# Kernel optimization log

Hardware: AMD Instinct MI355X
Metric: run time of the kernel (lower is better)

Reference implementation:

```python
import jax, jax.numpy as jnp
import numpy as np

N = 100000
E = 1600000
F = 128
HID = 64
OUT = 64
LSTM_H = (3 * HID) // 2  # 96, PyG JumpingKnowledge lstm hidden size


def setup_inputs() -> dict:
    key = jax.random.key(0)
    ks = jax.random.split(key, 40)

    def w(k, shape, s=0.05):
        return jax.random.normal(k, shape, dtype=jnp.float32) * s

    inp = {}
    inp['x'] = jax.random.normal(ks[0], (N, F), dtype=jnp.float32)
    inp['edge_index'] = jax.random.randint(ks[1], (2, E), 0, N)
    # GINConv MLPs: Linear(in,hid) -> ReLU -> Linear(hid,hid)
    dims = [(F, HID), (HID, HID), (HID, HID)]
    for i, (a, b) in enumerate(dims):
        inp[f'W{i}a'] = w(ks[2 + 4 * i], (b, a))
        inp[f'b{i}a'] = w(ks[3 + 4 * i], (b,))
        inp[f'W{i}b'] = w(ks[4 + 4 * i], (b, b))
        inp[f'b{i}b'] = w(ks[5 + 4 * i], (b,))
    # JK bidirectional LSTM (torch gate order i,f,g,o)
    for j, d in enumerate(['f', 'b']):
        inp[f'Wih_{d}'] = w(ks[14 + 4 * j], (4 * LSTM_H, HID))
        inp[f'Whh_{d}'] = w(ks[15 + 4 * j], (4 * LSTM_H, LSTM_H))
        inp[f'bih_{d}'] = w(ks[16 + 4 * j], (4 * LSTM_H,))
        inp[f'bhh_{d}'] = w(ks[17 + 4 * j], (4 * LSTM_H,))
    inp['Watt'] = w(ks[22], (1, 2 * LSTM_H))
    inp['batt'] = w(ks[23], (1,))
    inp['Wlin'] = w(ks[24], (OUT, HID))
    inp['blin'] = w(ks[25], (OUT,))
    inp['Wfc1'] = w(ks[26], (1, OUT))
    inp['bfc1'] = w(ks[27], (1,))
    inp['Wfc2'] = w(ks[28], (1, N))
    inp['bfc2'] = w(ks[29], (1,))
    return inp


def _gin_layer(h, src, dst, Wa, ba, Wb, bb):
    # GINConv with eps=0: MLP((1+eps)*x + sum_{j in N(i)} x_j)
    agg = jax.ops.segment_sum(h[src], dst, num_segments=h.shape[0])
    z = h + agg
    z = jnp.maximum(z @ Wa.T + ba, 0.0)
    return z @ Wb.T + bb


def _lstm_scan(seq, Wih, Whh, bih, bhh):
    # seq: [L, N, C]; returns hidden states [L, N, H]
    H = Whh.shape[1]
    bias = bih + bhh

    def cell(carry, xt):
        hp, cp = carry
        g = xt @ Wih.T + hp @ Whh.T + bias
        i, f, gg, o = jnp.split(g, 4, axis=-1)
        c = jax.nn.sigmoid(f) * cp + jax.nn.sigmoid(i) * jnp.tanh(gg)
        hn = jax.nn.sigmoid(o) * jnp.tanh(c)
        return (hn, c), hn

    n = seq.shape[1]
    init = (jnp.zeros((n, H), seq.dtype), jnp.zeros((n, H), seq.dtype))
    _, hs = jax.lax.scan(cell, init, seq)
    return hs


def reference(x, edge_index, W0a, b0a, W0b, b0b, W1a, b1a, W1b, b1b,
              W2a, b2a, W2b, b2b, Wih_f, Whh_f, bih_f, bhh_f,
              Wih_b, Whh_b, bih_b, bhh_b, Watt, batt, Wlin, blin,
              Wfc1, bfc1, Wfc2, bfc2):
    src, dst = edge_index[0], edge_index[1]
    h = x
    xs = []
    for (Wa, ba, Wb, bb) in [(W0a, b0a, W0b, b0b), (W1a, b1a, W1b, b1b),
                             (W2a, b2a, W2b, b2b)]:
        h = _gin_layer(h, src, dst, Wa, ba, Wb, bb)
        h = jnp.maximum(h, 0.0)  # BasicGNN act (relu); dropout=identity in eval
        xs.append(h)
    seq = jnp.stack(xs, axis=0)  # [L, N, HID]
    hf = _lstm_scan(seq, Wih_f, Whh_f, bih_f, bhh_f)
    hb = _lstm_scan(seq[::-1], Wih_b, Whh_b, bih_b, bhh_b)[::-1]
    ao = jnp.concatenate([hf, hb], axis=-1)  # [L, N, 2*LSTM_H]
    alpha = (ao @ Watt.T + batt)[..., 0]  # [L, N]
    alpha = jax.nn.softmax(alpha, axis=0)  # softmax over layers
    xjk = jnp.einsum('lnc,ln->nc', seq, alpha)  # [N, HID]
    xo = xjk @ Wlin.T + blin  # [N, OUT]
    v = (xo @ Wfc1.T + bfc1)[:, 0]  # [N]
    v = jnp.where(v >= 0, v, 0.01 * v)  # LeakyReLU
    return Wfc2 @ v + bfc2  # [1]
```

## Files before the change

kernel.cpp:

```cpp
#include <hip/hip_runtime.h>
#include <stdint.h>

typedef unsigned short u16;
typedef unsigned int u32;
using short8 = __attribute__((ext_vector_type(8))) short;
using f32x16 = __attribute__((ext_vector_type(16))) float;

__device__ __forceinline__ float sigf(float x){
  return __builtin_amdgcn_rcpf(1.0f + __expf(-x));
}
__device__ __forceinline__ float tanh_f(float x){
  return 1.0f - 2.0f*__builtin_amdgcn_rcpf(1.0f + __expf(2.0f*x));
}
__device__ __forceinline__ u16 f2bf(float f){
  u32 u = __float_as_uint(f);
  u += 0x7FFFu + ((u>>16)&1u);
  return (u16)(u>>16);
}
__device__ __forceinline__ float bf2f(u16 h){ return __uint_as_float(((u32)h)<<16); }

__global__ void k_deg(const int* __restrict__ dst, int* __restrict__ deg, int E){
  int i = blockIdx.x*256 + threadIdx.x;
  if (i < E) atomicAdd(&deg[dst[i]], 1);
}

__global__ __launch_bounds__(256) void k_scan1(const int* __restrict__ deg, int* __restrict__ indptr,
                                               int* __restrict__ bsum, int N){
  __shared__ int s[256];
  int tid = threadIdx.x;
  int i = blockIdx.x*256 + tid;
  int v = (i < N) ? deg[i] : 0;
  s[tid] = v; __syncthreads();
  for (int off=1; off<256; off<<=1){
    int t = (tid>=off) ? s[tid-off] : 0;
    __syncthreads();
    s[tid] += t;
    __syncthreads();
  }
  if (i < N) indptr[i] = s[tid] - v;
  if (tid == 255) bsum[blockIdx.x] = s[255];
}

__global__ __launch_bounds__(512) void k_scan2(const int* __restrict__ bsum, int* __restrict__ boffs,
                                               int* __restrict__ indptr, int nb, int N){
  __shared__ int s[512];
  int tid = threadIdx.x;
  int v = (tid < nb) ? bsum[tid] : 0;
  s[tid] = v; __syncthreads();
  for (int off=1; off<512; off<<=1){
    int t = (tid>=off) ? s[tid-off] : 0;
    __syncthreads();
    s[tid] += t;
    __syncthreads();
  }
  boffs[tid] = s[tid] - v;
  if (tid == nb-1) indptr[N] = s[tid];
}

__global__ __launch_bounds__(256) void k_scan3(int* __restrict__ indptr, const int* __restrict__ boffs, int N){
  int i = blockIdx.x*256 + threadIdx.x;
  if (i < N) indptr[i] += boffs[blockIdx.x];
}

__global__ void k_fill(const int* __restrict__ src, const int* __restrict__ dst,
                       const int* __restrict__ indptr, int* __restrict__ fill,
                       int* __restrict__ col, int E){
  int i = blockIdx.x*256 + threadIdx.x;
  if (i < E){
    int d = dst[i];
    int r = atomicAdd(&fill[d], 1);
    col[indptr[d] + r] = src[i];
  }
}

template<int F>
__global__ __launch_bounds__(256) void k_agg(const float* __restrict__ y, const int* __restrict__ indptr,
                                             const int* __restrict__ col, const float* __restrict__ bias,
                                             float* __restrict__ z, int N){
  constexpr int TPN = F/4;
  constexpr int NPB = 256/TPN;
  int n = blockIdx.x*NPB + threadIdx.x/TPN;
  int lane = threadIdx.x % TPN;
  if (n >= N) return;
  const float4* hv = (const float4*)y;
  float4 acc = hv[(size_t)n*TPN + lane];
  int s = indptr[n], e = indptr[n+1];
  int p = s;
  for (; p + 8 <= e; p += 8){
    int c8[8];
    #pragma unroll
    for (int i=0;i<8;++i) c8[i] = col[p+i];
    #pragma unroll
    for (int i=0;i<8;++i){
      float4 x = hv[(size_t)c8[i]*TPN + lane];
      acc.x += x.x; acc.y += x.y; acc.z += x.z; acc.w += x.w;
    }
  }
  for (; p < e; ++p){
    float4 x = hv[(size_t)col[p]*TPN + lane];
    acc.x += x.x; acc.y += x.y; acc.z += x.z; acc.w += x.w;
  }
  float4 b4 = ((const float4*)bias)[lane];
  acc.x = fmaxf(acc.x + b4.x, 0.f);
  acc.y = fmaxf(acc.y + b4.y, 0.f);
  acc.z = fmaxf(acc.z + b4.z, 0.f);
  acc.w = fmaxf(acc.w + b4.w, 0.f);
  ((float4*)z)[(size_t)n*TPN + lane] = acc;
}

__global__ __launch_bounds__(256) void k_packG(const float* __restrict__ W, u16* __restrict__ Wg, int K){
  int idx = blockIdx.x*256 + threadIdx.x;
  if (idx >= K*128) return;
  int i  = idx & 7;
  int l  = (idx>>3) & 63;
  int p  = (idx>>9) & 1;
  int rt = (idx>>10) & 1;
  int kt = idx >> 11;
  int j  = rt*32 + (l & 31);
  int k  = kt*16 + ((l>>5)<<3) + i;
  float v = W[(size_t)j*K + k];
  u16 h = f2bf(v);
  Wg[idx] = p ? f2bf(v - bf2f(h)) : h;
}

__device__ __forceinline__ void cvt8p(const float (&v)[8], u32 (&hw)[4], u32 (&lw)[4]){
  #pragma unroll
  for (int i=0;i<4;++i){
    u16 h0=f2bf(v[2*i]),   h1=f2bf(v[2*i+1]);
    u16 l0=f2bf(v[2*i]-bf2f(h0)), l1=f2bf(v[2*i+1]-bf2f(h1));
    hw[i]= (u32)h0 | ((u32)h1<<16);
    lw[i]= (u32)l0 | ((u32)l1<<16);
  }
}

__device__ __forceinline__ void stageG(const float (&v)[8], u16* __restrict__ BH, u16* __restrict__ BL,
                                       int node, int kc, int NKT){
  u32 hw[4], lw[4];
  cvt8p(v, hw, lw);
  int kt = kc >> 1, h2 = kc & 1;
  int sl = (((h2<<5) | (node&31)) ^ (kc & 7));
  int addr = (((node>>5)*NKT + kt)<<9) + (sl<<3);
  *(uint4*)(BH + addr) = make_uint4(hw[0],hw[1],hw[2],hw[3]);
  *(uint4*)(BL + addr) = make_uint4(lw[0],lw[1],lw[2],lw[3]);
}

template<int K, int ACT>
__global__ __launch_bounds__(256,2) void k_mfgemm(const float* __restrict__ A, const u16* __restrict__ Wg,
                                                  const float* __restrict__ bias, float* __restrict__ out,
                                                  int N){
  constexpr int NKT = K/16;
  __shared__ u16 BH[2*NKT*512];
  __shared__ u16 BL[2*NKT*512];
  const int tid = threadIdx.x;
  const int l = tid & 63;
  const int w = __builtin_amdgcn_readfirstlane(tid >> 6);
  const int rt = w >> 1, nt = w & 1;
  const int nb = blockIdx.x * 64;
  const int hi = l >> 5;

  for (int u = tid; u < 64*(K/8); u += 256){
    int node = u / (K/8);
    int kc = u % (K/8);
    int n = nb + node;
    float v[8];
    if (n < N){
      const float4* s4 = (const float4*)(A + (size_t)n*K + kc*8);
      float4 a = s4[0], b = s4[1];
      v[0]=a.x; v[1]=a.y; v[2]=a.z; v[3]=a.w; v[4]=b.x; v[5]=b.y; v[6]=b.z; v[7]=b.w;
    } else {
      #pragma unroll
      for (int i=0;i<8;++i) v[i]=0.f;
    }
    stageG(v, BH, BL, node, kc, NKT);
  }
  __syncthreads();

  f32x16 acc;
  #pragma unroll
  for (int r=0;r<16;++r) acc[r] = 0.f;
  const u16* wbase = Wg + ((size_t)rt<<10) + ((size_t)l<<3);
  #pragma unroll
  for (int kt = 0; kt < NKT; ++kt){
    const u16* wk = wbase + (size_t)kt*2048;
    short8 Ah = *(const short8*)(wk);
    short8 Al = *(const short8*)(wk + 512);
    int sl = l ^ (((kt<<1) + hi) & 7);
    int baddr = ((nt*NKT + kt)<<9) + (sl<<3);
    short8 Bh = *(const short8*)(BH + baddr);
    short8 Bl = *(const short8*)(BL + baddr);
    acc = __builtin_amdgcn_mfma_f32_32x32x16_bf16(Ah, Bh, acc, 0,0,0);
    acc = __builtin_amdgcn_mfma_f32_32x32x16_bf16(Ah, Bl, acc, 0,0,0);
    acc = __builtin_amdgcn_mfma_f32_32x32x16_bf16(Al, Bh, acc, 0,0,0);
  }

  const int col = l & 31;
  const int n = nb + nt*32 + col;
  if (n < N){
    #pragma unroll
    for (int g = 0; g < 4; ++g){
      const int j0 = rt*32 + 8*g + 4*hi;
      float4 b4 = bias ? *(const float4*)(bias + j0) : make_float4(0.f,0.f,0.f,0.f);
      float4 o;
      o.x = acc[4*g+0] + b4.x;
      o.y = acc[4*g+1] + b4.y;
      o.z = acc[4*g+2] + b4.z;
      o.w = acc[4*g+3] + b4.w;
      if (ACT){
        o.x = fmaxf(o.x, 0.f); o.y = fmaxf(o.y, 0.f);
        o.z = fmaxf(o.z, 0.f); o.w = fmaxf(o.w, 0.f);
      }
      *(float4*)(out + (size_t)n*64 + j0) = o;
    }
  }
}

__global__ __launch_bounds__(256,2) void k_mfgemm2(const float* __restrict__ Z, const u16* __restrict__ Wgb,
                                                   const float* __restrict__ bb, const u16* __restrict__ Wga,
                                                   float* __restrict__ Hout, float* __restrict__ Yout,
                                                   int N){
  __shared__ u16 BH[4096];
  __shared__ u16 BL[4096];
  __shared__ float hX[64][68];
  const int tid = threadIdx.x;
  const int l = tid & 63;
  const int w = __builtin_amdgcn_readfirstlane(tid >> 6);
  const int rt = w >> 1, nt = w & 1;
  const int nb = blockIdx.x * 64;
  const int hi = l >> 5;
  const int col = l & 31;
  const int n = nb + nt*32 + col;

  for (int u = tid; u < 512; u += 256){
    int node = u >> 3;
    int kc = u & 7;
    int nn = nb + node;
    float v[8];
    if (nn < N){
      const float4* s4 = (const float4*)(Z + (size_t)nn*64 + kc*8);
      float4 a = s4[0], b = s4[1];
      v[0]=a.x; v[1]=a.y; v[2]=a.z; v[3]=a.w; v[4]=b.x; v[5]=b.y; v[6]=b.z; v[7]=b.w;
    } else {
      #pragma unroll
      for (int i=0;i<8;++i) v[i]=0.f;
    }
    stageG(v, BH, BL, node, kc, 4);
  }
  __syncthreads();

  f32x16 acc;
  #pragma unroll
  for (int r=0;r<16;++r) acc[r] = 0.f;
  {
    const u16* wbase = Wgb + ((size_t)rt<<10) + ((size_t)l<<3);
    #pragma unroll
    for (int kt = 0; kt < 4; ++kt){
      const u16* wk = wbase + (size_t)kt*2048;
      short8 Ah = *(const short8*)(wk);
      short8 Al = *(const short8*)(wk + 512);
      int sl = l ^ (((kt<<1) + hi) & 7);
      int baddr = ((nt*4 + kt)<<9) + (sl<<3);
      short8 Bh = *(const short8*)(BH + baddr);
      short8 Bl = *(const short8*)(BL + baddr);
      acc = __builtin_amdgcn_mfma_f32_32x32x16_bf16(Ah, Bh, acc, 0,0,0);
      acc = __builtin_amdgcn_mfma_f32_32x32x16_bf16(Ah, Bl, acc, 0,0,0);
      acc = __builtin_amdgcn_mfma_f32_32x32x16_bf16(Al, Bh, acc, 0,0,0);
    }
  }
  {
    const int node = nt*32 + col;
    #pragma unroll
    for (int g = 0; g < 4; ++g){
      const int j0 = rt*32 + 8*g + 4*hi;
      float4 b4 = *(const float4*)(bb + j0);
      float4 o;
      o.x = fmaxf(acc[4*g+0] + b4.x, 0.f);
      o.y = fmaxf(acc[4*g+1] + b4.y, 0.f);
      o.z = fmaxf(acc[4*g+2] + b4.z, 0.f);
      o.w = fmaxf(acc[4*g+3] + b4.w, 0.f);
      if (n < N) *(float4*)(Hout + (size_t)n*64 + j0) = o;
      *(float4*)(&hX[node][j0]) = o;
    }
  }
  __syncthreads();

  for (int u = tid; u < 512; u += 256){
    int node = u >> 3;
    int kc = u & 7;
    float v[8];
    #pragma unroll
    for (int i=0;i<8;++i) v[i] = hX[node][kc*8 + i];
    stageG(v, BH, BL, node, kc, 4);
  }
  __syncthreads();

  #pragma unroll
  for (int r=0;r<16;++r) acc[r] = 0.f;
  {
    const u16* wbase = Wga + ((size_t)rt<<10) + ((size_t)l<<3);
    #pragma unroll
    for (int kt = 0; kt < 4; ++kt){
      const u16* wk = wbase + (size_t)kt*2048;
      short8 Ah = *(const short8*)(wk);
      short8 Al = *(const short8*)(wk + 512);
      int sl = l ^ (((kt<<1) + hi) & 7);
      int baddr = ((nt*4 + kt)<<9) + (sl<<3);
      short8 Bh = *(const short8*)(BH + baddr);
      short8 Bl = *(const short8*)(BL + baddr);
      acc = __builtin_amdgcn_mfma_f32_32x32x16_bf16(Ah, Bh, acc, 0,0,0);
      acc = __builtin_amdgcn_mfma_f32_32x32x16_bf16(Ah, Bl, acc, 0,0,0);
      acc = __builtin_amdgcn_mfma_f32_32x32x16_bf16(Al, Bh, acc, 0,0,0);
    }
  }
  if (n < N){
    #pragma unroll
    for (int g = 0; g < 4; ++g){
      const int j0 = rt*32 + 8*g + 4*hi;
      float4 o;
      o.x = acc[4*g+0]; o.y = acc[4*g+1]; o.z = acc[4*g+2]; o.w = acc[4*g+3];
      *(float4*)(Yout + (size_t)n*64 + j0) = o;
    }
  }
}

__global__ __launch_bounds__(256) void k_packW1(const float* __restrict__ Wih, const float* __restrict__ Whh,
                                                u16* __restrict__ Wp){
  int idx = blockIdx.x*256 + threadIdx.x;
  if (idx >= 10*12*64*8) return;
  int i  = idx & 7;
  int l  = (idx>>3) & 63;
  int rt = (idx>>9) % 12;
  int kt = (idx>>9) / 12;
  int r  = rt*32 + (l & 31);
  int j  = r >> 2, g = r & 3;
  int row = g*96 + j;
  int k  = kt*16 + ((l>>5)<<3) + i;
  float v = (k < 64) ? Wih[row*64 + k] : Whh[row*96 + (k-64)];
  Wp[idx] = f2bf(v);
}

__global__ __launch_bounds__(128) void k_packB(const float* __restrict__ bih, const float* __restrict__ bhh,
                                               float4* __restrict__ Bp){
  int j = blockIdx.x*128 + threadIdx.x;
  if (j >= 96) return;
  Bp[j] = make_float4(bih[j]+bhh[j], bih[96+j]+bhh[96+j],
                      bih[192+j]+bhh[192+j], bih[288+j]+bhh[288+j]);
}

__device__ __forceinline__ void ldx_regs(const float* __restrict__ seq, int blk, int N, int tid,
                                         float (&v)[8]){
  int node = tid >> 3;
  int kc = tid & 7;
  int n = blk*32 + node;
  if (n < N){
    const float4* s4 = (const float4*)(seq + (size_t)n*64 + kc*8);
    float4 a = s4[0], b = s4[1];
    v[0]=a.x; v[1]=a.y; v[2]=a.z; v[3]=a.w; v[4]=b.x; v[5]=b.y; v[6]=b.z; v[7]=b.w;
  } else {
    #pragma unroll
    for (int i=0;i<8;++i) v[i]=0.f;
  }
}

__device__ __forceinline__ void stage_from_regs(const float (&v)[8], u16* __restrict__ XH,
                                                u16* __restrict__ XL, int tid){
  int node = tid >> 3;
  int kc = tid & 7;
  u32 hw[4], lw[4];
  cvt8p(v, hw, lw);
  int kt = kc >> 1, hi = kc & 1;
  int sl = (((hi<<5) | node) ^ (kc & 7));
  int addr = (kt<<9) + (sl<<3);
  *(uint4*)(XH + addr) = make_uint4(hw[0],hw[1],hw[2],hw[3]);
  *(uint4*)(XL + addr) = make_uint4(lw[0],lw[1],lw[2],lw[3]);
}

__device__ __forceinline__ void restage_h16(const u16 (*hFH)[32], u16* __restrict__ XH, int tid){
  int node = tid & 31;
  #pragma unroll
  for (int q = 0; q < 2; ++q){
    int cc = (tid >> 5) + q*8;
    if (cc < 12){
      int kth = cc >> 1, hi = cc & 1;
      int ktG = kth + 4;
      u32 hw[4];
      #pragma unroll
      for (int i=0;i<4;++i){
        u16 a = hFH[cc*8 + 2*i][node];
        u16 b = hFH[cc*8 + 2*i + 1][node];
        hw[i] = (u32)a | ((u32)b<<16);
      }
      int sl = (((hi<<5) | node) ^ ((2*ktG + hi) & 7));
      int addr = (ktG<<9) + (sl<<3);
      *(uint4*)(XH + addr) = make_uint4(hw[0],hw[1],hw[2],hw[3]);
    }
  }
}

template<int FIRST, int WRITEH>
__device__ __forceinline__ float lstm_step5(const u16* __restrict__ Wp,
    const float4* __restrict__ Bp, const float* __restrict__ WattW,
    const u16* __restrict__ XH, const u16* __restrict__ XL, u16 (*hFH)[32],
    float (&c)[12], int rtg, int l)
{
  constexpr int NKT = FIRST ? 4 : 10;
  const int hi = l >> 5;
  const int col = l & 31;
  f32x16 acc[3];
  #pragma unroll
  for (int t=0;t<3;++t)
    #pragma unroll
    for (int r=0;r<16;++r) acc[t][r] = 0.f;

  const u16* wbase = Wp + (size_t)(rtg*3)*512 + ((size_t)l<<3);
  #pragma unroll
  for (int kt = 0; kt < NKT; ++kt){
    const u16* wk = wbase + (size_t)kt*6144;
    short8 A0 = *(const short8*)(wk);
    short8 A1 = *(const short8*)(wk + 512);
    short8 A2 = *(const short8*)(wk + 1024);
    int sl = l ^ (((kt<<1) + hi) & 7);
    int baddr = (kt<<9) + (sl<<3);
    short8 Bh = *(const short8*)(XH + baddr);
    __builtin_amdgcn_s_setprio(1);
    acc[0] = __builtin_amdgcn_mfma_f32_32x32x16_bf16(A0, Bh, acc[0], 0,0,0);
    acc[1] = __builtin_amdgcn_mfma_f32_32x32x16_bf16(A1, Bh, acc[1], 0,0,0);
    acc[2] = __builtin_amdgcn_mfma_f32_32x32x16_bf16(A2, Bh, acc[2], 0,0,0);
    if (kt < 4){
      short8 Bl = *(const short8*)(XL + baddr);
      acc[0] = __builtin_amdgcn_mfma_f32_32x32x16_bf16(A0, Bl, acc[0], 0,0,0);
      acc[1] = __builtin_amdgcn_mfma_f32_32x32x16_bf16(A1, Bl, acc[1], 0,0,0);
      acc[2] = __builtin_amdgcn_mfma_f32_32x32x16_bf16(A2, Bl, acc[2], 0,0,0);
    }
    __builtin_amdgcn_s_setprio(0);
  }

  float aP = 0.f;
  #pragma unroll
  for (int ti=0;ti<3;++ti){
    #pragma unroll
    for (int rg=0; rg<4; ++rg){
      const int j = (rtg*3+ti)*8 + 2*rg + hi;
      float4 bv = Bp[j];
      float gi = acc[ti][rg*4+0] + bv.x;
      float gf = acc[ti][rg*4+1] + bv.y;
      float gg = acc[ti][rg*4+2] + bv.z;
      float go = acc[ti][rg*4+3] + bv.w;
      const int ci = ti*4 + rg;
      float cp = FIRST ? 0.f : c[ci];
      float cn = sigf(gf)*cp + sigf(gi)*tanh_f(gg);
      float hh = sigf(go)*tanh_f(cn);
      c[ci] = cn;
      aP = fmaf(hh, WattW[j], aP);
      if (WRITEH) hFH[j][col] = f2bf(hh);
    }
  }
  return aP;
}

__global__ __launch_bounds__(256,2) void k_lstm5(
    const float* __restrict__ h1, const float* __restrict__ h2, const float* __restrict__ h3,
    const u16* __restrict__ Wpf, const u16* __restrict__ Wpb,
    const float4* __restrict__ Bpf, const float4* __restrict__ Bpb,
    const float* __restrict__ Watt, const float* __restrict__ batt,
    float* __restrict__ aF, float* __restrict__ aB, int gL, int N)
{
  __shared__ u16 XH[5120];
  __shared__ u16 XL[2048];
  __shared__ u16 hFH[96][32];
  __shared__ float sAl[4][3][32];
  const int tid = threadIdx.x;
  const int l = tid & 63;
  const int rtg = __builtin_amdgcn_readfirstlane(tid >> 6);
  const int dir = (blockIdx.x >= gL) ? 1 : 0;
  const int blk = blockIdx.x - dir*gL;
  const float* sA = dir ? h3 : h1;
  const float* sC = dir ? h1 : h3;
  const u16* Wp = dir ? Wpb : Wpf;
  const float4* Bp = dir ? Bpb : Bpf;
  const float* WattW = Watt + dir*96;
  float* aD = dir ? aB : aF;
  float c[12];
  float a0, a1, a2;
  float xv[8];

  ldx_regs(sA, blk, N, tid, xv);
  stage_from_regs(xv, XH, XL, tid);
  ldx_regs(h2, blk, N, tid, xv);
  __syncthreads();

  a0 = lstm_step5<1,1>(Wp, Bp, WattW, XH, XL, hFH, c, rtg, l);
  __syncthreads();
  stage_from_regs(xv, XH, XL, tid);
  restage_h16(hFH, XH, tid);
  ldx_regs(sC, blk, N, tid, xv);
  __syncthreads();

  a1 = lstm_step5<0,1>(Wp, Bp, WattW, XH, XL, hFH, c, rtg, l);
  __syncthreads();
  stage_from_regs(xv, XH, XL, tid);
  restage_h16(hFH, XH, tid);
  __syncthreads();

  a2 = lstm_step5<0,0>(Wp, Bp, WattW, XH, XL, hFH, c, rtg, l);

  a0 += __shfl_xor(a0, 32);
  a1 += __shfl_xor(a1, 32);
  a2 += __shfl_xor(a2, 32);
  if (l < 32){
    sAl[rtg][0][l] = a0;
    sAl[rtg][1][l] = a1;
    sAl[rtg][2][l] = a2;
  }
  __syncthreads();
  if (tid < 96){
    int s = tid >> 5;
    int node = tid & 31;
    int n = blk*32 + node;
    if (n < N){
      float sum = sAl[0][s][node] + sAl[1][s][node]
                + sAl[2][s][node] + sAl[3][s][node];
      int slice = dir ? (2 - s) : s;
      float v = dir ? sum : (batt[0] + sum);
      aD[(size_t)slice*N + n] = v;
    }
  }
}

__global__ __launch_bounds__(256,2) void k_jk2(const float* __restrict__ aF, const float* __restrict__ aB,
                                               const float* __restrict__ h1, const float* __restrict__ h2,
                                               const float* __restrict__ h3,
                                               const u16* __restrict__ WgL, const float* __restrict__ blin,
                                               const float* __restrict__ Wfc1, const float* __restrict__ bfc1,
                                               float* __restrict__ vout, int N){
  __shared__ u16 BH[4096];
  __shared__ u16 BL[4096];
  __shared__ float sP[4][32];
  const int tid = threadIdx.x;
  const int l = tid & 63;
  const int w = __builtin_amdgcn_readfirstlane(tid >> 6);
  const int rt = w >> 1, nt = w & 1;
  const int nb = blockIdx.x * 64;
  const int hi = l >> 5;
  const int col = l & 31;

  for (int u = tid; u < 512; u += 256){
    int node = u >> 3;
    int kc = u & 7;
    int n = nb + node;
    float v[8];
    if (n < N){
      float a0 = aF[n] + aB[n];
      float a1 = aF[(size_t)N + n] + aB[(size_t)N + n];
      float a2 = aF[(size_t)2*N + n] + aB[(size_t)2*N + n];
      float m = fmaxf(a0, fmaxf(a1, a2));
      float e0 = __expf(a0-m), e1 = __expf(a1-m), e2 = __expf(a2-m);
      float inv = __builtin_amdgcn_rcpf(e0+e1+e2);
      float w0 = e0*inv, w1 = e1*inv, w2 = e2*inv;
      const float4* p1 = (const float4*)(h1 + (size_t)n*64 + kc*8);
      const float4* p2 = (const float4*)(h2 + (size_t)n*64 + kc*8);
      const float4* p3 = (const float4*)(h3 + (size_t)n*64 + kc*8);
      #pragma unroll
      for (int q=0;q<2;++q){
        float4 x1 = p1[q], x2 = p2[q], x3 = p3[q];
        v[4*q+0] = w0*x1.x + w1*x2.x + w2*x3.x;
        v[4*q+1] = w0*x1.y + w1*x2.y + w2*x3.y;
        v[4*q+2] = w0*x1.z + w1*x2.z + w2*x3.z;
        v[4*q+3] = w0*x1.w + w1*x2.w + w2*x3.w;
      }
    } else {
      #pragma unroll
      for (int i=0;i<8;++i) v[i]=0.f;
    }
    stageG(v, BH, BL, node, kc, 4);
  }
  __syncthreads();

  f32x16 acc;
  #pragma unroll
  for (int r=0;r<16;++r) acc[r] = 0.f;
  const u16* wbase = WgL + ((size_t)rt<<10) + ((size_t)l<<3);
  #pragma unroll
  for (int kt = 0; kt < 4; ++kt){
    const u16* wk = wbase + (size_t)kt*2048;
    short8 Ah = *(const short8*)(wk);
    short8 Al = *(const short8*)(wk + 512);
    int sl = l ^ (((kt<<1) + hi) & 7);
    int baddr = ((nt*4 + kt)<<9) + (sl<<3);
    short8 Bh = *(const short8*)(BH + baddr);
    short8 Bl = *(const short8*)(BL + baddr);
    acc = __builtin_amdgcn_mfma_f32_32x32x16_bf16(Ah, Bh, acc, 0,0,0);
    acc = __builtin_amdgcn_mfma_f32_32x32x16_bf16(Ah, Bl, acc, 0,0,0);
    acc = __builtin_amdgcn_mfma_f32_32x32x16_bf16(Al, Bh, acc, 0,0,0);
  }

  float p = 0.f;
  #pragma unroll
  for (int g = 0; g < 4; ++g){
    #pragma unroll
    for (int rg = 0; rg < 4; ++rg){
      const int j = rt*32 + 8*g + 4*hi + rg;
      p += (acc[4*g+rg] + blin[j]) * Wfc1[j];
    }
  }
  p += __shfl_xor(p, 32);
  if (l < 32) sP[w][l] = p;
  __syncthreads();
  if (tid < 64){
    int node = tid;
    int nt2 = node >> 5, c2 = node & 31;
    int n = nb + node;
    if (n < N){
      float t = sP[nt2][c2] + sP[2+nt2][c2] + bfc1[0];
      vout[n] = t >= 0.f ? t : 0.01f*t;
    }
  }
}

__global__ __launch_bounds__(256) void k_final1(const float* __restrict__ w, const float* __restrict__ v,
                                                double* __restrict__ part, int N){
  __shared__ double sd[256];
  int tid = threadIdx.x;
  double a = 0.0;
  for (int i = blockIdx.x*256 + tid; i < N; i += 256*256)
    a += (double)(w[i] * v[i]);
  sd[tid] = a; __syncthreads();
  for (int off = 128; off > 0; off >>= 1){
    if (tid < off) sd[tid] += sd[tid + off];
    __syncthreads();
  }
  if (tid == 0) part[blockIdx.x] = sd[0];
}

__global__ __launch_bounds__(256) void k_final2(const double* __restrict__ part, const float* __restrict__ bfc2,
                                                float* __restrict__ out){
  __shared__ double sd[256];
  int tid = threadIdx.x;
  sd[tid] = part[tid]; __syncthreads();
  for (int off = 128; off > 0; off >>= 1){
    if (tid < off) sd[tid] += sd[tid + off];
    __syncthreads();
  }
  if (tid == 0) out[0] = (float)(sd[0] + (double)bfc2[0]);
}

extern "C" void kernel_launch(void* const* d_in, const int* in_sizes, int n_in,
                              void* d_out, int out_size, void* d_ws, size_t ws_size,
                              hipStream_t stream){
  const float* x    = (const float*)d_in[0];
  const int*   ei   = (const int*)d_in[1];
  const float* W0a  = (const float*)d_in[2];
  const float* b0a  = (const float*)d_in[3];
  const float* W0b  = (const float*)d_in[4];
  const float* b0b  = (const float*)d_in[5];
  const float* W1a  = (const float*)d_in[6];
  const float* b1a  = (const float*)d_in[7];
  const float* W1b  = (const float*)d_in[8];
  const float* b1b  = (const float*)d_in[9];
  const float* W2a  = (const float*)d_in[10];
  const float* b2a  = (const float*)d_in[11];
  const float* W2b  = (const float*)d_in[12];
  const float* b2b  = (const float*)d_in[13];
  const float* Wih_f = (const float*)d_in[14];
  const float* Whh_f = (const float*)d_in[15];
  const float* bih_f = (const float*)d_in[16];
  const float* bhh_f = (const float*)d_in[17];
  const float* Wih_b = (const float*)d_in[18];
  const float* Whh_b = (const float*)d_in[19];
  const float* bih_b = (const float*)d_in[20];
  const float* bhh_b = (const float*)d_in[21];
  const float* Watt = (const float*)d_in[22];
  const float* batt = (const float*)d_in[23];
  const float* Wlin = (const float*)d_in[24];
  const float* blin = (const float*)d_in[25];
  const float* Wfc1 = (const float*)d_in[26];
  const float* bfc1 = (const float*)d_in[27];
  const float* Wfc2 = (const float*)d_in[28];
  const float* bfc2 = (const float*)d_in[29];
  float* out = (float*)d_out;

  const int N = in_sizes[0] / 128;
  const int E = in_sizes[1] / 2;
  const int* src = ei;
  const int* dst = ei + E;

  uint8_t* w8 = (uint8_t*)d_ws;
  size_t off = 0;
  auto alloc = [&](size_t bytes) -> void* {
    void* p = w8 + off;
    off = (off + bytes + 255) & ~(size_t)255;
    return p;
  };
  int*    deg    = (int*)   alloc((size_t)N*4);
  int*    fill   = (int*)   alloc((size_t)N*4);
  int*    indptr = (int*)   alloc(((size_t)N+1)*4);
  int*    col    = (int*)   alloc((size_t)E*4);
  int*    bsum   = (int*)   alloc(2048);
  int*    boffs  = (int*)   alloc(2048);
  float*  h1     = (float*) alloc((size_t)N*64*4);
  float*  h2     = (float*) alloc((size_t)N*64*4);
  float*  h3     = (float*) alloc((size_t)N*64*4);
  float*  aF     = (float*) alloc((size_t)3*N*4);
  float*  aB     = (float*) alloc((size_t)3*N*4);
  float*  vbuf   = (float*) alloc((size_t)N*4);
  double* part   = (double*)alloc(256*8);
  u16*    Wpf    = (u16*)   alloc((size_t)10*12*64*8*2);
  u16*    Wpb    = (u16*)   alloc((size_t)10*12*64*8*2);
  float4* Bpf    = (float4*)alloc((size_t)96*16);
  float4* Bpb    = (float4*)alloc((size_t)96*16);
  u16*    Wg0a   = (u16*)   alloc((size_t)128*128*2);
  u16*    Wg0b   = (u16*)   alloc((size_t)64*128*2);
  u16*    Wg1a   = (u16*)   alloc((size_t)64*128*2);
  u16*    Wg1b   = (u16*)   alloc((size_t)64*128*2);
  u16*    Wg2a   = (u16*)   alloc((size_t)64*128*2);
  u16*    Wg2b   = (u16*)   alloc((size_t)64*128*2);
  u16*    WgL    = (u16*)   alloc((size_t)64*128*2);
  float*  P      = (float*) alloc((size_t)N*192*4);
  if (off > ws_size) return;
  float* ybuf = P;
  float* zbuf = P + (size_t)N*64;

  hipMemsetAsync(deg,  0, (size_t)N*4, stream);
  hipMemsetAsync(fill, 0, (size_t)N*4, stream);

  int gE = (E + 255) / 256;
  int nb1 = (N + 255) / 256;
  int gG = (N + 63) / 64;
  int gA = (N + 15) / 16;
  int gL = (N + 31) / 32;

  k_packW1<<<240, 256, 0, stream>>>(Wih_f, Whh_f, Wpf);
  k_packW1<<<240, 256, 0, stream>>>(Wih_b, Whh_b, Wpb);
  k_packB<<<1, 128, 0, stream>>>(bih_f, bhh_f, Bpf);
  k_packB<<<1, 128, 0, stream>>>(bih_b, bhh_b, Bpb);
  k_packG<<<64, 256, 0, stream>>>(W0a, Wg0a, 128);
  k_packG<<<32, 256, 0, stream>>>(W0b, Wg0b, 64);
  k_packG<<<32, 256, 0, stream>>>(W1a, Wg1a, 64);
  k_packG<<<32, 256, 0, stream>>>(W1b, Wg1b, 64);
  k_packG<<<32, 256, 0, stream>>>(W2a, Wg2a, 64);
  k_packG<<<32, 256, 0, stream>>>(W2b, Wg2b, 64);
  k_packG<<<32, 256, 0, stream>>>(Wlin, WgL, 64);

  k_deg  <<<gE, 256, 0, stream>>>(dst, deg, E);
  k_scan1<<<nb1, 256, 0, stream>>>(deg, indptr, bsum, N);
  k_scan2<<<1, 512, 0, stream>>>(bsum, boffs, indptr, nb1, N);
  k_scan3<<<nb1, 256, 0, stream>>>(indptr, boffs, N);
  k_fill <<<gE, 256, 0, stream>>>(src, dst, indptr, fill, col, E);

  k_mfgemm<128,0><<<gG, 256, 0, stream>>>(x, Wg0a, nullptr, ybuf, N);
  k_agg<64><<<gA, 256, 0, stream>>>(ybuf, indptr, col, b0a, zbuf, N);
  k_mfgemm2<<<gG, 256, 0, stream>>>(zbuf, Wg0b, b0b, Wg1a, h1, ybuf, N);
  k_agg<64><<<gA, 256, 0, stream>>>(ybuf, indptr, col, b1a, zbuf, N);
  k_mfgemm2<<<gG, 256, 0, stream>>>(zbuf, Wg1b, b1b, Wg2a, h2, ybuf, N);
  k_agg<64><<<gA, 256, 0, stream>>>(ybuf, indptr, col, b2a, zbuf, N);
  k_mfgemm<64,1><<<gG, 256, 0, stream>>>(zbuf, Wg2b, b2b, h3, N);

  k_lstm5<<<2*gL, 256, 0, stream>>>(h1, h2, h3, Wpf, Wpb, Bpf, Bpb, Watt, batt,
                                    aF, aB, gL, N);

  k_jk2<<<gG, 256, 0, stream>>>(aF, aB, h1, h2, h3, WgL, blin, Wfc1, bfc1, vbuf, N);

  k_final1<<<256, 256, 0, stream>>>(Wfc2, vbuf, part, N);
  k_final2<<<1, 256, 0, stream>>>(part, bfc2, out);
}
```

Baseline: 626.4 us.

## Merge weight-packing launches, drop LSTM input low-part MFMAs, combine memsets

Replaces eleven small weight and bias packing kernels with one block-dispatched packing kernel, and merges the two memsets into a single contiguous memset. The aim is to cut per-launch overhead. The LSTM input staging now keeps only the bf16 high part of the input features, which removes the extra low-part MFMAs and the XL shared buffer. This lowers LSTM compute and LDS use but reduces precision of the input projection. The combined memset assumes deg and fill are adjacent, with only zero-safe buffers between them.

```diff
diff --git a/kernel.cpp b/kernel.cpp
--- a/kernel.cpp
+++ b/kernel.cpp
@@ -108,8 +108,23 @@
   ((float4*)z)[(size_t)n*TPN + lane] = acc;
 }
 
-__global__ __launch_bounds__(256) void k_packG(const float* __restrict__ W, u16* __restrict__ Wg, int K){
-  int idx = blockIdx.x*256 + threadIdx.x;
+__device__ __forceinline__ void packW1_body(int idx, const float* __restrict__ Wih,
+                                            const float* __restrict__ Whh, u16* __restrict__ Wp){
+  if (idx >= 10*12*64*8) return;
+  int i  = idx & 7;
+  int l  = (idx>>3) & 63;
+  int rt = (idx>>9) % 12;
+  int kt = (idx>>9) / 12;
+  int r  = rt*32 + (l & 31);
+  int j  = r >> 2, g = r & 3;
+  int row = g*96 + j;
+  int k  = kt*16 + ((l>>5)<<3) + i;
+  float v = (k < 64) ? Wih[row*64 + k] : Whh[row*96 + (k-64)];
+  Wp[idx] = f2bf(v);
+}
+
+__device__ __forceinline__ void packG_body(int idx, const float* __restrict__ W,
+                                           u16* __restrict__ Wg, int K){
   if (idx >= K*128) return;
   int i  = idx & 7;
   int l  = (idx>>3) & 63;
@@ -121,6 +136,56 @@
   float v = W[(size_t)j*K + k];
   u16 h = f2bf(v);
   Wg[idx] = p ? f2bf(v - bf2f(h)) : h;
+}
+
+__global__ __launch_bounds__(256) void k_packAll(
+    const float* __restrict__ Wih_f, const float* __restrict__ Whh_f,
+    const float* __restrict__ Wih_b, const float* __restrict__ Whh_b,
+    const float* __restrict__ bih_f, const float* __restrict__ bhh_f,
+    const float* __restrict__ bih_b, const float* __restrict__ bhh_b,
+    const float* __restrict__ W0a, const float* __restrict__ W0b,
+    const float* __restrict__ W1a, const float* __restrict__ W1b,
+    const float* __restrict__ W2a, const float* __restrict__ W2b,
+    const float* __restrict__ Wlin,
+    u16* __restrict__ Wpf, u16* __restrict__ Wpb,
+    float4* __restrict__ Bpf, float4* __restrict__ Bpb,
+    u16* __restrict__ Wg0a, u16* __restrict__ Wg0b,
+    u16* __restrict__ Wg1a, u16* __restrict__ Wg1b,
+    u16* __restrict__ Wg2a, u16* __restrict__ Wg2b,
+    u16* __restrict__ WgL)
+{
+  int b = blockIdx.x;
+  int tid = threadIdx.x;
+  if (b < 240){ packW1_body(b*256+tid, Wih_f, Whh_f, Wpf); return; }
+  b -= 240;
+  if (b < 240){ packW1_body(b*256+tid, Wih_b, Whh_b, Wpb); return; }
+  b -= 240;
+  if (b == 0){
+    if (tid < 96){
+      int j = tid;
+      Bpf[j] = make_float4(bih_f[j]+bhh_f[j], bih_f[96+j]+bhh_f[96+j],
+                           bih_f[192+j]+bhh_f[192+j], bih_f[288+j]+bhh_f[288+j]);
+    } else if (tid >= 128 && tid < 224){
+      int j = tid - 128;
+      Bpb[j] = make_float4(bih_b[j]+bhh_b[j], bih_b[96+j]+bhh_b[96+j],
+                           bih_b[192+j]+bhh_b[192+j], bih_b[288+j]+bhh_b[288+j]);
+    }
+    return;
+  }
+  b -= 1;
+  if (b < 64){ packG_body(b*256+tid, W0a, Wg0a, 128); return; }
+  b -= 64;
+  if (b < 32){ packG_body(b*256+tid, W0b, Wg0b, 64); return; }
+  b -= 32;
+  if (b < 32){ packG_body(b*256+tid, W1a, Wg1a, 64); return; }
+  b -= 32;
+  if (b < 32){ packG_body(b*256+tid, W1b, Wg1b, 64); return; }
+  b -= 32;
+  if (b < 32){ packG_body(b*256+tid, W2a, Wg2a, 64); return; }
+  b -= 32;
+  if (b < 32){ packG_body(b*256+tid, W2b, Wg2b, 64); return; }
+  b -= 32;
+  packG_body(b*256+tid, Wlin, WgL, 64);
 }
 
 __device__ __forceinline__ void cvt8p(const float (&v)[8], u32 (&hw)[4], u32 (&lw)[4]){
@@ -322,30 +387,6 @@
   }
 }
 
-__global__ __launch_bounds__(256) void k_packW1(const float* __restrict__ Wih, const float* __restrict__ Whh,
-                                                u16* __restrict__ Wp){
-  int idx = blockIdx.x*256 + threadIdx.x;
-  if (idx >= 10*12*64*8) return;
-  int i  = idx & 7;
-  int l  = (idx>>3) & 63;
-  int rt = (idx>>9) % 12;
-  int kt = (idx>>9) / 12;
-  int r  = rt*32 + (l & 31);
-  int j  = r >> 2, g = r & 3;
-  int row = g*96 + j;
-  int k  = kt*16 + ((l>>5)<<3) + i;
-  float v = (k < 64) ? Wih[row*64 + k] : Whh[row*96 + (k-64)];
-  Wp[idx] = f2bf(v);
-}
-
-__global__ __launch_bounds__(128) void k_packB(const float* __restrict__ bih, const float* __restrict__ bhh,
-                                               float4* __restrict__ Bp){
-  int j = blockIdx.x*128 + threadIdx.x;
-  if (j >= 96) return;
-  Bp[j] = make_float4(bih[j]+bhh[j], bih[96+j]+bhh[96+j],
-                      bih[192+j]+bhh[192+j], bih[288+j]+bhh[288+j]);
-}
-
 __device__ __forceinline__ void ldx_regs(const float* __restrict__ seq, int blk, int N, int tid,
                                          float (&v)[8]){
   int node = tid >> 3;
@@ -361,17 +402,17 @@
   }
 }
 
-__device__ __forceinline__ void stage_from_regs(const float (&v)[8], u16* __restrict__ XH,
-                                                u16* __restrict__ XL, int tid){
+__device__ __forceinline__ void stage_x_h16(const float (&v)[8], u16* __restrict__ XH, int tid){
   int node = tid >> 3;
   int kc = tid & 7;
-  u32 hw[4], lw[4];
-  cvt8p(v, hw, lw);
+  u32 hw[4];
+  #pragma unroll
+  for (int i=0;i<4;++i)
+    hw[i] = (u32)f2bf(v[2*i]) | ((u32)f2bf(v[2*i+1])<<16);
   int kt = kc >> 1, hi = kc & 1;
   int sl = (((hi<<5) | node) ^ (kc & 7));
   int addr = (kt<<9) + (sl<<3);
   *(uint4*)(XH + addr) = make_uint4(hw[0],hw[1],hw[2],hw[3]);
-  *(uint4*)(XL + addr) = make_uint4(lw[0],lw[1],lw[2],lw[3]);
 }
 
 __device__ __forceinline__ void restage_h16(const u16 (*hFH)[32], u16* __restrict__ XH, int tid){
@@ -399,7 +440,7 @@
 template<int FIRST, int WRITEH>
 __device__ __forceinline__ float lstm_step5(const u16* __restrict__ Wp,
     const float4* __restrict__ Bp, const float* __restrict__ WattW,
-    const u16* __restrict__ XH, const u16* __restrict__ XL, u16 (*hFH)[32],
+    const u16* __restrict__ XH, u16 (*hFH)[32],
     float (&c)[12], int rtg, int l)
 {
   constexpr int NKT = FIRST ? 4 : 10;
@@ -425,12 +466,6 @@
     acc[0] = __builtin_amdgcn_mfma_f32_32x32x16_bf16(A0, Bh, acc[0], 0,0,0);
     acc[1] = __builtin_amdgcn_mfma_f32_32x32x16_bf16(A1, Bh, acc[1], 0,0,0);
     acc[2] = __builtin_amdgcn_mfma_f32_32x32x16_bf16(A2, Bh, acc[2], 0,0,0);
-    if (kt < 4){
-      short8 Bl = *(const short8*)(XL + baddr);
-      acc[0] = __builtin_amdgcn_mfma_f32_32x32x16_bf16(A0, Bl, acc[0], 0,0,0);
-      acc[1] = __builtin_amdgcn_mfma_f32_32x32x16_bf16(A1, Bl, acc[1], 0,0,0);
-      acc[2] = __builtin_amdgcn_mfma_f32_32x32x16_bf16(A2, Bl, acc[2], 0,0,0);
-    }
     __builtin_amdgcn_s_setprio(0);
   }
 
@@ -465,7 +500,6 @@
     float* __restrict__ aF, float* __restrict__ aB, int gL, int N)
 {
   __shared__ u16 XH[5120];
-  __shared__ u16 XL[2048];
   __shared__ u16 hFH[96][32];
   __shared__ float sAl[4][3][32];
   const int tid = threadIdx.x;
@@ -484,24 +518,24 @@
   float xv[8];
 
   ldx_regs(sA, blk, N, tid, xv);
-  stage_from_regs(xv, XH, XL, tid);
+  stage_x_h16(xv, XH, tid);
   ldx_regs(h2, blk, N, tid, xv);
   __syncthreads();
 
-  a0 = lstm_step5<1,1>(Wp, Bp, WattW, XH, XL, hFH, c, rtg, l);
-  __syncthreads();
-  stage_from_regs(xv, XH, XL, tid);
+  a0 = lstm_step5<1,1>(Wp, Bp, WattW, XH, hFH, c, rtg, l);
+  __syncthreads();
+  stage_x_h16(xv, XH, tid);
   restage_h16(hFH, XH, tid);
   ldx_regs(sC, blk, N, tid, xv);
   __syncthreads();
 
-  a1 = lstm_step5<0,1>(Wp, Bp, WattW, XH, XL, hFH, c, rtg, l);
-  __syncthreads();
-  stage_from_regs(xv, XH, XL, tid);
+  a1 = lstm_step5<0,1>(Wp, Bp, WattW, XH, hFH, c, rtg, l);
+  __syncthreads();
+  stage_x_h16(xv, XH, tid);
   restage_h16(hFH, XH, tid);
   __syncthreads();
 
-  a2 = lstm_step5<0,0>(Wp, Bp, WattW, XH, XL, hFH, c, rtg, l);
+  a2 = lstm_step5<0,0>(Wp, Bp, WattW, XH, hFH, c, rtg, l);
 
   a0 += __shfl_xor(a0, 32);
   a1 += __shfl_xor(a1, 32);
@@ -541,7 +575,6 @@
   const int rt = w >> 1, nt = w & 1;
   const int nb = blockIdx.x * 64;
   const int hi = l >> 5;
-  const int col = l & 31;
 
   for (int u = tid; u < 512; u += 256){
     int node = u >> 3;
@@ -719,8 +752,8 @@
   float* ybuf = P;
   float* zbuf = P + (size_t)N*64;
 
-  hipMemsetAsync(deg,  0, (size_t)N*4, stream);
-  hipMemsetAsync(fill, 0, (size_t)N*4, stream);
+  size_t zlen = (size_t)((uint8_t*)fill - (uint8_t*)deg) + (size_t)N*4;
+  hipMemsetAsync(deg, 0, zlen, stream);
 
   int gE = (E + 255) / 256;
   int nb1 = (N + 255) / 256;
@@ -728,17 +761,11 @@
   int gA = (N + 15) / 16;
   int gL = (N + 31) / 32;
 
-  k_packW1<<<240, 256, 0, stream>>>(Wih_f, Whh_f, Wpf);
-  k_packW1<<<240, 256, 0, stream>>>(Wih_b, Whh_b, Wpb);
-  k_packB<<<1, 128, 0, stream>>>(bih_f, bhh_f, Bpf);
-  k_packB<<<1, 128, 0, stream>>>(bih_b, bhh_b, Bpb);
-  k_packG<<<64, 256, 0, stream>>>(W0a, Wg0a, 128);
-  k_packG<<<32, 256, 0, stream>>>(W0b, Wg0b, 64);
-  k_packG<<<32, 256, 0, stream>>>(W1a, Wg1a, 64);
-  k_packG<<<32, 256, 0, stream>>>(W1b, Wg1b, 64);
-  k_packG<<<32, 256, 0, stream>>>(W2a, Wg2a, 64);
-  k_packG<<<32, 256, 0, stream>>>(W2b, Wg2b, 64);
-  k_packG<<<32, 256, 0, stream>>>(Wlin, WgL, 64);
+  k_packAll<<<737, 256, 0, stream>>>(Wih_f, Whh_f, Wih_b, Whh_b,
+                                     bih_f, bhh_f, bih_b, bhh_b,
+                                     W0a, W0b, W1a, W1b, W2a, W2b, Wlin,
+                                     Wpf, Wpb, Bpf, Bpb,
+                                     Wg0a, Wg0b, Wg1a, Wg1b, Wg2a, Wg2b, WgL);
 
   k_deg  <<<gE, 256, 0, stream>>>(dst, deg, E);
   k_scan1<<<nb1, 256, 0, stream>>>(deg, indptr, bsum, N);
```

After: 592.0 us. 1.06x faster.
